# Optimization experiments

Hardware: AMD Instinct MI355X
Metric: run time of the kernel (lower is better)

The kernel has to match this reference:

```python
import jax, jax.numpy as jnp
import numpy as np

B, S, D, H = 2, 2048, 2048, 16
DH = D // H
FF = 4 * D
EPS = 1e-5


def setup_inputs() -> dict:
    key = jax.random.key(0)
    ks = jax.random.split(key, 8)
    sd = 0.02
    return {
        "hidden_states": jax.random.normal(ks[0], (B, S, D), jnp.float32),
        "ln1_w": jnp.ones((D,), jnp.float32),
        "ln1_b": jnp.zeros((D,), jnp.float32),
        "qkv_w": jax.random.normal(ks[1], (3 * D, D), jnp.float32) * sd,
        "qkv_b": jnp.zeros((3 * D,), jnp.float32),
        "dense_w": jax.random.normal(ks[2], (D, D), jnp.float32) * sd,
        "dense_b": jnp.zeros((D,), jnp.float32),
        "ln2_w": jnp.ones((D,), jnp.float32),
        "ln2_b": jnp.zeros((D,), jnp.float32),
        "fc1_w": jax.random.normal(ks[3], (FF, D), jnp.float32) * sd,
        "fc1_b": jnp.zeros((FF,), jnp.float32),
        "fc2_w": jax.random.normal(ks[4], (D, FF), jnp.float32) * sd,
        "fc2_b": jnp.zeros((D,), jnp.float32),
    }


def _layer_norm(x, w, b):
    mu = jnp.mean(x, axis=-1, keepdims=True)
    var = jnp.mean(jnp.square(x - mu), axis=-1, keepdims=True)
    return (x - mu) * jax.lax.rsqrt(var + EPS) * w + b


def _attention(x, qkv_w, qkv_b, dense_w, dense_b):
    qkv = x @ qkv_w.T + qkv_b  # [B,S,3D]
    q, k, v = jnp.split(qkv, 3, axis=-1)
    q = q.reshape(B, S, H, DH)
    k = k.reshape(B, S, H, DH)
    v = v.reshape(B, S, H, DH)
    scale = DH ** -0.5
    scores = jnp.einsum("bqhd,bkhd->bhqk", q, k) * scale
    causal = jnp.tril(jnp.ones((S, S), bool))
    scores = jnp.where(causal, scores, jnp.finfo(scores.dtype).min)
    probs = jax.nn.softmax(scores, axis=-1)
    out = jnp.einsum("bhqk,bkhd->bqhd", probs, v).reshape(B, S, D)
    return out @ dense_w.T + dense_b


def reference(hidden_states, ln1_w, ln1_b, qkv_w, qkv_b, dense_w, dense_b,
              ln2_w, ln2_b, fc1_w, fc1_b, fc2_w, fc2_b):
    residual = hidden_states
    x = _layer_norm(hidden_states, ln1_w, ln1_b)
    x = _attention(x, qkv_w, qkv_b, dense_w, dense_b) + residual
    residual = x
    h = _layer_norm(x, ln2_w, ln2_b)
    h = jax.nn.gelu(h @ fc1_w.T + fc1_b, approximate=False)
    h = h @ fc2_w.T + fc2_b
    return residual + h
```

## Files before the change

### kernel.cpp

```cpp
#include <hip/hip_runtime.h>
#include <hip/hip_bf16.h>

#define SEQ    2048
#define DMODEL 2048
#define NHEAD  16
#define DHEAD  128
#define TOK    4096
#define TD     6144
#define FFDIM  8192

typedef __attribute__((ext_vector_type(4)))  float f32x4;
typedef __attribute__((ext_vector_type(16))) float f32x16;
typedef __attribute__((ext_vector_type(8)))  short short8v;

__device__ __forceinline__ void async_ld16(const void* src, void* lds) {
  __builtin_amdgcn_global_load_lds((const __attribute__((address_space(1))) void*)src,
                                   (__attribute__((address_space(3))) void*)lds, 16, 0, 0);
}

__device__ __forceinline__ unsigned pk2(float a, float b) {
  union { __hip_bfloat16 h[2]; unsigned u; } p;
  p.h[0] = __float2bfloat16(a);
  p.h[1] = __float2bfloat16(b);
  return p.u;
}

__global__ __launch_bounds__(256) void f2bf_kernel(const float* __restrict__ in,
                                                   __hip_bfloat16* __restrict__ out, long n) {
  long i0 = ((long)blockIdx.x * 256 + threadIdx.x) * 8;
  long stride = (long)gridDim.x * 256 * 8;
  for (long i = i0; i < n; i += stride) {
    float4 a = *(const float4*)(in + i);
    float4 b = *(const float4*)(in + i + 4);
    union { __hip_bfloat16 h[8]; int4 v; } p;
    p.h[0] = __float2bfloat16(a.x); p.h[1] = __float2bfloat16(a.y);
    p.h[2] = __float2bfloat16(a.z); p.h[3] = __float2bfloat16(a.w);
    p.h[4] = __float2bfloat16(b.x); p.h[5] = __float2bfloat16(b.y);
    p.h[6] = __float2bfloat16(b.z); p.h[7] = __float2bfloat16(b.w);
    *(int4*)(out + i) = p.v;
  }
}

__global__ __launch_bounds__(256) void ln_kernel(const float* __restrict__ x,
                                                 const float* __restrict__ w,
                                                 const float* __restrict__ b,
                                                 __hip_bfloat16* __restrict__ out) {
  __shared__ float red[8];
  const int row = blockIdx.x;
  const int tid = threadIdx.x;
  const float* xr = x + (long)row * DMODEL;
  float4 v0 = ((const float4*)xr)[tid * 2];
  float4 v1 = ((const float4*)xr)[tid * 2 + 1];
  float s  = v0.x + v0.y + v0.z + v0.w + v1.x + v1.y + v1.z + v1.w;
  float ss = v0.x*v0.x + v0.y*v0.y + v0.z*v0.z + v0.w*v0.w
           + v1.x*v1.x + v1.y*v1.y + v1.z*v1.z + v1.w*v1.w;
  #pragma unroll
  for (int m = 1; m < 64; m <<= 1) { s += __shfl_xor(s, m, 64); ss += __shfl_xor(ss, m, 64); }
  if ((tid & 63) == 0) { red[tid >> 6] = s; red[4 + (tid >> 6)] = ss; }
  __syncthreads();
  s  = red[0] + red[1] + red[2] + red[3];
  ss = red[4] + red[5] + red[6] + red[7];
  const float mu = s * (1.0f / DMODEL);
  const float rs = rsqrtf(ss * (1.0f / DMODEL) - mu * mu + 1e-5f);
  float4 w0 = ((const float4*)w)[tid * 2], w1 = ((const float4*)w)[tid * 2 + 1];
  float4 b0 = ((const float4*)b)[tid * 2], b1 = ((const float4*)b)[tid * 2 + 1];
  union { __hip_bfloat16 h[8]; int4 v; } p;
  p.h[0] = __float2bfloat16((v0.x - mu) * rs * w0.x + b0.x);
  p.h[1] = __float2bfloat16((v0.y - mu) * rs * w0.y + b0.y);
  p.h[2] = __float2bfloat16((v0.z - mu) * rs * w0.z + b0.z);
  p.h[3] = __float2bfloat16((v0.w - mu) * rs * w0.w + b0.w);
  p.h[4] = __float2bfloat16((v1.x - mu) * rs * w1.x + b1.x);
  p.h[5] = __float2bfloat16((v1.y - mu) * rs * w1.y + b1.y);
  p.h[6] = __float2bfloat16((v1.z - mu) * rs * w1.z + b1.z);
  p.h[7] = __float2bfloat16((v1.w - mu) * rs * w1.w + b1.w);
  ((int4*)(out + (long)row * DMODEL))[tid] = p.v;
}

#define VMBAR(N) asm volatile("s_waitcnt vmcnt(" #N ")\ns_barrier" ::: "memory")
#define LGK(N)   do { asm volatile("s_waitcnt lgkmcnt(" #N ")" ::: "memory"); \
                      __builtin_amdgcn_sched_barrier(0); } while (0)

#define RA_READ_A(DST, BB, MH) \
  _Pragma("unroll") \
  for (int m = 0; m < 4; ++m) { \
    int row = wr * 128 + (MH) * 64 + m * 16 + l15; \
    _Pragma("unroll") \
    for (int kk = 0; kk < 2; ++kk) \
      DST[m][kk] = *(const short8v*)((BB) + row * 128 + ((((kk << 2) | c16) ^ (row & 7)) << 4)); \
  }
#define RA_READ_B(DST, BB) \
  _Pragma("unroll") \
  for (int n = 0; n < 2; ++n) { \
    int row = wc * 32 + n * 16 + l15; \
    _Pragma("unroll") \
    for (int kk = 0; kk < 2; ++kk) \
      DST[n][kk] = *(const short8v*)((BB) + 32768 + row * 128 + ((((kk << 2) | c16) ^ (row & 7)) << 4)); \
  }
#define RA_MFMA(AF, BF, MH) \
  __builtin_amdgcn_s_setprio(1); \
  _Pragma("unroll") \
  for (int m = 0; m < 4; ++m) \
    _Pragma("unroll") \
    for (int n = 0; n < 2; ++n) \
      _Pragma("unroll") \
      for (int kk = 0; kk < 2; ++kk) \
        acc[(MH) * 4 + m][n] = __builtin_amdgcn_mfma_f32_16x16x32_bf16( \
            AF[m][kk], BF[n][kk], acc[(MH) * 4 + m][n], 0, 0, 0); \
  __builtin_amdgcn_s_setprio(0);

template <int MODE>
__global__ __launch_bounds__(512, 2) void gemm128ra(const __hip_bfloat16* __restrict__ A,
                                                    const __hip_bfloat16* __restrict__ B,
                                                    const float* __restrict__ bias,
                                                    const float* __restrict__ resid,
                                                    void* __restrict__ outp,
                                                    int N, long K) {
  __shared__ __align__(16) char lds[98304];
  const int tid = threadIdx.x;
  const int lane = tid & 63, w = tid >> 6;
  const int wr = w >> 2, wc = w & 3;
  const int l15 = lane & 15, c16 = lane >> 4;
  const int gx = gridDim.x;
  const int nwg = gx * (int)gridDim.y;
  const int lin = (int)blockIdx.y * gx + (int)blockIdx.x;
  const int cpx = nwg >> 3;
  const int swz = (lin & 7) * cpx + (lin >> 3);
  const long m0 = (long)(swz / gx) * 256;
  const long n0 = (long)(swz % gx) * 128;
  const int NT = (int)(K >> 6);
  const int NI = NT >> 1;

  auto stA2 = [&](int t, int par) {
    char* base = lds + (t & 1) * 49152;
    #pragma unroll
    for (int j = 0; j < 2; ++j) {
      int q = 2 * j + par;
      int row = q * 64 + (tid >> 3);
      long col = (long)t * 64 + (((tid & 7) ^ (row & 7)) << 3);
      async_ld16(A + (m0 + row) * K + col, base + q * 8192 + w * 1024);
    }
  };
  auto stB1 = [&](int t) {
    char* base = lds + (t & 1) * 49152 + 32768;
    #pragma unroll
    for (int j = 0; j < 2; ++j) {
      int row = j * 64 + (tid >> 3);
      long col = (long)t * 64 + (((tid & 7) ^ (row & 7)) << 3);
      async_ld16(B + (n0 + row) * K + col, base + j * 8192 + w * 1024);
    }
  };

  f32x4 acc[8][2] = {};
  short8v afA[4][2], afB[4][2], bfA[2][2], bfB[2][2];
  const char* b0 = lds;
  const char* b1 = lds + 49152;

  stB1(0); stA2(0, 0); stA2(0, 1);
  stB1(1); stA2(1, 0);
  asm volatile("s_waitcnt vmcnt(4)\ns_barrier" ::: "memory");
  RA_READ_A(afA, b0, 0); RA_READ_B(bfA, b0);

  for (int i = 0; i < NI; ++i) {
    const bool last = (i == NI - 1);
    const int c = 2 * i + 1, e = 2 * i + 2, g = 2 * i + 3;

    VMBAR(4);
    RA_READ_A(afB, b0, 1);
    stA2(c, 1);
    LGK(8);
    RA_MFMA(afA, bfA, 0);

    VMBAR(2);
    RA_READ_A(afA, b1, 0);
    RA_READ_B(bfB, b1);
    if (!last) { stB1(e); stA2(e, 0); }
    LGK(12);
    RA_MFMA(afB, bfA, 1);

    if (!last) { VMBAR(4); } else { VMBAR(0); }
    RA_READ_A(afB, b1, 1);
    if (!last) stA2(e, 1);
    LGK(8);
    RA_MFMA(afA, bfB, 0);

    if (!last) {
      VMBAR(2);
      RA_READ_A(afA, b0, 0);
      RA_READ_B(bfA, b0);
      stB1(g); stA2(g, 0);
      LGK(12);
    } else {
      LGK(0);
    }
    RA_MFMA(afB, bfB, 1);
  }

  const int colq = l15;
  const int rowq = c16 * 4;
  #pragma unroll
  for (int n = 0; n < 2; ++n) {
    long col = n0 + wc * 32 + n * 16 + colq;
    float bi = bias[col];
    #pragma unroll
    for (int mi = 0; mi < 8; ++mi) {
      long row0 = m0 + wr * 128 + mi * 16 + rowq;
      #pragma unroll
      for (int j = 0; j < 4; ++j) {
        long idx = (row0 + j) * (long)N + col;
        float v = acc[mi][n][j] + bi;
        if (MODE == 0) {
          ((__hip_bfloat16*)outp)[idx] = __float2bfloat16(v);
        } else if (MODE == 1) {
          ((float*)outp)[idx] = v + resid[idx];
        } else {
          float g = 0.5f * v * (1.0f + erff(v * 0.70710678118654752f));
          ((__hip_bfloat16*)outp)[idx] = __float2bfloat16(g);
        }
      }
    }
  }
}

#define QBLK 128
#define KVB  64
#define VSTR 144
#define KBYT 16384
#define VBYT (DHEAD * VSTR)
__global__ __launch_bounds__(256, 2) void attn_kernel(const __hip_bfloat16* __restrict__ qkv,
                                                      __hip_bfloat16* __restrict__ out) {
  __shared__ __align__(16) char smem[2 * KBYT + 2 * VBYT];
  const int tid = threadIdx.x, lane = tid & 63, wid = tid >> 6;
  const int l31 = lane & 31, hi = lane >> 5;
  const int bx = blockIdx.x;
  const int bh = blockIdx.y;
  const int bb = bh >> 4, h = bh & 15;
  const long rowbase = (long)bb * SEQ;
  const int qcol = h * DHEAD, kcol = DMODEL + h * DHEAD, vcol = 2 * DMODEL + h * DHEAD;

  const int kv0s = (tid >> 4) * 4;
  const int dh0s = (tid & 15) * 8;
  auto k_stage = [&](int t) {
    char* kb = smem + (t & 1) * KBYT;
    const long kvr = rowbase + (long)t * KVB;
    #pragma unroll
    for (int i = 0; i < 4; ++i) {
      int c = i * 256 + tid;
      int row = c >> 4, slot = c & 15;
      const void* src = qkv + (kvr + row) * TD + kcol + ((slot ^ (row & 7)) << 3);
      async_ld16(src, kb + i * 4096 + wid * 1024);
    }
  };
  auto v_load = [&](int t, int4* r) {
    const long kvr = rowbase + (long)t * KVB;
    #pragma unroll
    for (int i = 0; i < 4; ++i)
      r[i] = *(const int4*)(qkv + (kvr + kv0s + i) * TD + vcol + dh0s);
  };
  auto v_write = [&](int t, const int4* r) {
    char* vt = smem + 2 * KBYT + (t & 1) * VBYT;
    union { int4 v; unsigned short s[8]; } u0, u1, u2, u3;
    u0.v = r[0]; u1.v = r[1]; u2.v = r[2]; u3.v = r[3];
    #pragma unroll
    for (int dd = 0; dd < 8; ++dd) {
      int d = (dd + ((tid >> 1) & 7)) & 7;
      unsigned lo = (unsigned)u0.s[d] | ((unsigned)u1.s[d] << 16);
      unsigned hi2 = (unsigned)u2.s[d] | ((unsigned)u3.s[d] << 16);
      uint2 wv; wv.x = lo; wv.y = hi2;
      *(uint2*)(vt + (dh0s + d) * VSTR + kv0s * 2) = wv;
    }
  };

  #pragma unroll
  for (int mem = 0; mem < 2; ++mem) {
    const int qb = mem == 0 ? (15 - bx) : bx;
    const int q0 = qb * QBLK;
    const int qw0 = q0 + wid * 32;

    short8v qf[8];
    {
      const __hip_bfloat16* qp = qkv + (rowbase + qw0 + l31) * TD + qcol + hi * 8;
      #pragma unroll
      for (int kc = 0; kc < 8; ++kc) qf[kc] = *(const short8v*)(qp + kc * 16);
    }

    f32x16 o[4] = {};
    float m_ = -1e30f, l_ = 0.0f;
    const int nt = (q0 + QBLK) / KVB;

    {
      int4 vr[4];
      v_load(0, vr);
      k_stage(0);
      v_write(0, vr);
    }
    __syncthreads();

    for (int t = 0; t < nt; ++t) {
      int4 vr[4];
      const bool more = (t + 1 < nt);
      if (more) { v_load(t + 1, vr); k_stage(t + 1); }

      const int kv0 = t * KVB;
      if (kv0 <= qw0 + 31) {
        const char* Kb = smem + (t & 1) * KBYT;
        f32x16 s0 = {}, s1 = {};
        #pragma unroll
        for (int kc = 0; kc < 8; ++kc) {
          const int colb = kc * 32 + hi * 16;
          const int r0 = l31, r1 = 32 + l31;
          short8v k0 = *(const short8v*)(Kb + r0 * 256 + (colb ^ ((r0 & 7) << 4)));
          short8v k1 = *(const short8v*)(Kb + r1 * 256 + (colb ^ ((r0 & 7) << 4)));
          s0 = __builtin_amdgcn_mfma_f32_32x32x16_bf16(k0, qf[kc], s0, 0, 0, 0);
          s1 = __builtin_amdgcn_mfma_f32_32x32x16_bf16(k1, qf[kc], s1, 0, 0, 0);
        }
        const float scale = 0.08838834764831845f;
        float sv[32];
        #pragma unroll
        for (int r = 0; r < 16; ++r) { sv[r] = s0[r] * scale; sv[16 + r] = s1[r] * scale; }
        const int qg = qw0 + l31;
        if (kv0 + KVB - 1 > qw0) {
          #pragma unroll
          for (int r = 0; r < 16; ++r) {
            int kvr_ = kv0 + (r & 3) + 8 * (r >> 2) + 4 * hi;
            if (kvr_ > qg)      sv[r]      = -1e30f;
            if (kvr_ + 32 > qg) sv[16 + r] = -1e30f;
          }
        }
        float pmax = sv[0];
        #pragma unroll
        for (int r = 1; r < 32; ++r) pmax = fmaxf(pmax, sv[r]);
        pmax = fmaxf(pmax, __shfl_xor(pmax, 32, 64));
        float mn = fmaxf(m_, pmax);
        float alpha = __expf(m_ - mn);
        m_ = mn;
        l_ *= alpha;
        #pragma unroll
        for (int d = 0; d < 4; ++d)
          #pragma unroll
          for (int r = 0; r < 16; ++r) o[d][r] *= alpha;
        float rsum = 0.0f;
        #pragma unroll
        for (int r = 0; r < 32; ++r) { sv[r] = __expf(sv[r] - m_); rsum += sv[r]; }
        l_ += rsum + __shfl_xor(rsum, 32, 64);
        int pa_[4][4];
        #pragma unroll
        for (int kc = 0; kc < 4; ++kc) {
          int ba = 16 * (kc >> 1) + 8 * (kc & 1);
          unsigned wA0 = pk2(sv[ba + 0], sv[ba + 1]);
          unsigned wA1 = pk2(sv[ba + 2], sv[ba + 3]);
          unsigned wB0 = pk2(sv[ba + 4], sv[ba + 5]);
          unsigned wB1 = pk2(sv[ba + 6], sv[ba + 7]);
          unsigned z0 = (unsigned)__shfl_xor((int)(hi ? wA0 : wB0), 32, 64);
          unsigned z1 = (unsigned)__shfl_xor((int)(hi ? wA1 : wB1), 32, 64);
          pa_[kc][0] = hi ? (int)z0 : (int)wA0;
          pa_[kc][1] = hi ? (int)z1 : (int)wA1;
          pa_[kc][2] = hi ? (int)wB0 : (int)z0;
          pa_[kc][3] = hi ? (int)wB1 : (int)z1;
        }
        const char* Vt = smem + 2 * KBYT + (t & 1) * VBYT;
        #pragma unroll
        for (int dht = 0; dht < 4; ++dht) {
          const int dh = dht * 32 + l31;
          short8v vf[4];
          #pragma unroll
          for (int kc = 0; kc < 4; ++kc)
            vf[kc] = *(const short8v*)(Vt + dh * VSTR + kc * 32 + hi * 16);
          #pragma unroll
          for (int kc = 0; kc < 4; ++kc) {
            union { int i[4]; short8v v; } bv;
            bv.i[0] = pa_[kc][0]; bv.i[1] = pa_[kc][1];
            bv.i[2] = pa_[kc][2]; bv.i[3] = pa_[kc][3];
            o[dht] = __builtin_amdgcn_mfma_f32_32x32x16_bf16(vf[kc], bv.v, o[dht], 0, 0, 0);
          }
        }
      }
      if (more) v_write(t + 1, vr);
      __syncthreads();
    }

    const float linv = 1.0f / l_;
    const long orow = (rowbase + qw0 + l31) * DMODEL + h * DHEAD;
    #pragma unroll
    for (int dht = 0; dht < 4; ++dht)
      #pragma unroll
      for (int rg = 0; rg < 4; ++rg) {
        union { __hip_bfloat16 hh[4]; uint2 u; } pk;
        #pragma unroll
        for (int i = 0; i < 4; ++i) pk.hh[i] = __float2bfloat16(o[dht][rg * 4 + i] * linv);
        *(uint2*)(out + orow + dht * 32 + 8 * rg + 4 * hi) = pk.u;
      }
  }
}

extern "C" void kernel_launch(void* const* d_in, const int* in_sizes, int n_in,
                              void* d_out, int out_size, void* d_ws, size_t ws_size,
                              hipStream_t stream) {
  const float* hidden  = (const float*)d_in[0];
  const float* ln1w    = (const float*)d_in[1];
  const float* ln1b    = (const float*)d_in[2];
  const float* qkvw    = (const float*)d_in[3];
  const float* qkvb    = (const float*)d_in[4];
  const float* densew  = (const float*)d_in[5];
  const float* denseb  = (const float*)d_in[6];
  const float* ln2w    = (const float*)d_in[7];
  const float* ln2b    = (const float*)d_in[8];
  const float* fc1w    = (const float*)d_in[9];
  const float* fc1b    = (const float*)d_in[10];
  const float* fc2w    = (const float*)d_in[11];
  const float* fc2b    = (const float*)d_in[12];

  char* ws = (char*)d_ws;
  size_t off = 0;
  auto alloc = [&](size_t bytes) { char* p = ws + off; off += (bytes + 255) & ~(size_t)255; return p; };
  __hip_bfloat16* xbf    = (__hip_bfloat16*)alloc((size_t)TOK * DMODEL * 2);
  __hip_bfloat16* wqkv   = (__hip_bfloat16*)alloc((size_t)TD * DMODEL * 2);
  __hip_bfloat16* wdense = (__hip_bfloat16*)alloc((size_t)DMODEL * DMODEL * 2);
  __hip_bfloat16* wfc1   = (__hip_bfloat16*)alloc((size_t)FFDIM * DMODEL * 2);
  __hip_bfloat16* wfc2   = (__hip_bfloat16*)alloc((size_t)DMODEL * FFDIM * 2);
  __hip_bfloat16* big    = (__hip_bfloat16*)alloc((size_t)TOK * FFDIM * 2);
  float*          x2     = (float*)alloc((size_t)TOK * DMODEL * 4);
  __hip_bfloat16* qkvbuf  = big;
  __hip_bfloat16* attnout = big + (size_t)TOK * TD;
  __hip_bfloat16* gelubuf = big;

  f2bf_kernel<<<1024, 256, 0, stream>>>(qkvw,   wqkv,   (long)TD * DMODEL);
  f2bf_kernel<<<1024, 256, 0, stream>>>(densew, wdense, (long)DMODEL * DMODEL);
  f2bf_kernel<<<1024, 256, 0, stream>>>(fc1w,   wfc1,   (long)FFDIM * DMODEL);
  f2bf_kernel<<<1024, 256, 0, stream>>>(fc2w,   wfc2,   (long)DMODEL * FFDIM);

  ln_kernel<<<TOK, 256, 0, stream>>>(hidden, ln1w, ln1b, xbf);
  gemm128ra<0><<<dim3(TD / 128, TOK / 256), 512, 0, stream>>>(xbf, wqkv, qkvb, nullptr, qkvbuf, TD, DMODEL);
  attn_kernel<<<dim3(8, 2 * NHEAD), 256, 0, stream>>>(qkvbuf, attnout);
  gemm128ra<1><<<dim3(DMODEL / 128, TOK / 256), 512, 0, stream>>>(attnout, wdense, denseb, hidden, x2, DMODEL, DMODEL);
  ln_kernel<<<TOK, 256, 0, stream>>>(x2, ln2w, ln2b, xbf);
  gemm128ra<2><<<dim3(FFDIM / 128, TOK / 256), 512, 0, stream>>>(xbf, wfc1, fc1b, nullptr, gelubuf, FFDIM, DMODEL);
  gemm128ra<1><<<dim3(DMODEL / 128, TOK / 256), 512, 0, stream>>>(gelubuf, wfc2, fc2b, x2, (float*)d_out, DMODEL, FFDIM);
}
```

Baseline: 656.9 us.

## Simplify GEMM pipeline to whole-tile double buffering with full vmcnt waits

Replaces the staggered half-tile prefetch schedule in the bf16 GEMM with a simpler double-buffer scheme. Each stage now waits for all outstanding global loads, issues the full next tile (B plus both A halves), then computes on the current buffer with a single B fragment set. This removes the interleaved partial waits and one register fragment set. In exchange, global loads overlap less finely with MFMA work, and the vmcnt(0) barriers may expose memory latency.

```diff
diff --git a/kernel.cpp b/kernel.cpp
--- a/kernel.cpp
+++ b/kernel.cpp
@@ -76,7 +76,7 @@
   ((int4*)(out + (long)row * DMODEL))[tid] = p.v;
 }
 
-#define VMBAR(N) asm volatile("s_waitcnt vmcnt(" #N ")\ns_barrier" ::: "memory")
+#define VMBAR0() asm volatile("s_waitcnt vmcnt(0)\ns_barrier" ::: "memory")
 #define LGK(N)   do { asm volatile("s_waitcnt lgkmcnt(" #N ")" ::: "memory"); \
                       __builtin_amdgcn_sched_barrier(0); } while (0)
 
@@ -109,7 +109,7 @@
   __builtin_amdgcn_s_setprio(0);
 
 template <int MODE>
-__global__ __launch_bounds__(512, 2) void gemm128ra(const __hip_bfloat16* __restrict__ A,
+__global__ __launch_bounds__(512, 2) void gemm128fr(const __hip_bfloat16* __restrict__ A,
                                                     const __hip_bfloat16* __restrict__ B,
                                                     const float* __restrict__ bias,
                                                     const float* __restrict__ resid,
@@ -151,48 +151,30 @@
   };
 
   f32x4 acc[8][2] = {};
-  short8v afA[4][2], afB[4][2], bfA[2][2], bfB[2][2];
+  short8v afA[4][2], afB[4][2], bfA[2][2];
   const char* b0 = lds;
   const char* b1 = lds + 49152;
 
   stB1(0); stA2(0, 0); stA2(0, 1);
-  stB1(1); stA2(1, 0);
-  asm volatile("s_waitcnt vmcnt(4)\ns_barrier" ::: "memory");
+  VMBAR0();
+  stB1(1); stA2(1, 0); stA2(1, 1);
   RA_READ_A(afA, b0, 0); RA_READ_B(bfA, b0);
 
   for (int i = 0; i < NI; ++i) {
-    const bool last = (i == NI - 1);
-    const int c = 2 * i + 1, e = 2 * i + 2, g = 2 * i + 3;
-
-    VMBAR(4);
     RA_READ_A(afB, b0, 1);
-    stA2(c, 1);
-    LGK(8);
-    RA_MFMA(afA, bfA, 0);
-
-    VMBAR(2);
-    RA_READ_A(afA, b1, 0);
-    RA_READ_B(bfB, b1);
-    if (!last) { stB1(e); stA2(e, 0); }
-    LGK(12);
-    RA_MFMA(afB, bfA, 1);
-
-    if (!last) { VMBAR(4); } else { VMBAR(0); }
+    LGK(8);  RA_MFMA(afA, bfA, 0);
+    LGK(0);  RA_MFMA(afB, bfA, 1);
+    VMBAR0();
+    if (2 * i + 2 < NT) { stB1(2 * i + 2); stA2(2 * i + 2, 0); stA2(2 * i + 2, 1); }
+    RA_READ_A(afA, b1, 0); RA_READ_B(bfA, b1);
     RA_READ_A(afB, b1, 1);
-    if (!last) stA2(e, 1);
-    LGK(8);
-    RA_MFMA(afA, bfB, 0);
-
-    if (!last) {
-      VMBAR(2);
-      RA_READ_A(afA, b0, 0);
-      RA_READ_B(bfA, b0);
-      stB1(g); stA2(g, 0);
-      LGK(12);
-    } else {
-      LGK(0);
-    }
-    RA_MFMA(afB, bfB, 1);
+    LGK(8);  RA_MFMA(afA, bfA, 0);
+    LGK(0);  RA_MFMA(afB, bfA, 1);
+    if (i + 1 < NI) {
+      VMBAR0();
+      stB1(2 * i + 3); stA2(2 * i + 3, 0); stA2(2 * i + 3, 1);
+      RA_READ_A(afA, b0, 0); RA_READ_B(bfA, b0);
+    }
   }
 
   const int colq = l15;
@@ -429,10 +411,10 @@
   f2bf_kernel<<<1024, 256, 0, stream>>>(fc2w,   wfc2,   (long)DMODEL * FFDIM);
 
   ln_kernel<<<TOK, 256, 0, stream>>>(hidden, ln1w, ln1b, xbf);
-  gemm128ra<0><<<dim3(TD / 128, TOK / 256), 512, 0, stream>>>(xbf, wqkv, qkvb, nullptr, qkvbuf, TD, DMODEL);
+  gemm128fr<0><<<dim3(TD / 128, TOK / 256), 512, 0, stream>>>(xbf, wqkv, qkvb, nullptr, qkvbuf, TD, DMODEL);
   attn_kernel<<<dim3(8, 2 * NHEAD), 256, 0, stream>>>(qkvbuf, attnout);
-  gemm128ra<1><<<dim3(DMODEL / 128, TOK / 256), 512, 0, stream>>>(attnout, wdense, denseb, hidden, x2, DMODEL, DMODEL);
+  gemm128fr<1><<<dim3(DMODEL / 128, TOK / 256), 512, 0, stream>>>(attnout, wdense, denseb, hidden, x2, DMODEL, DMODEL);
   ln_kernel<<<TOK, 256, 0, stream>>>(x2, ln2w, ln2b, xbf);
-  gemm128ra<2><<<dim3(FFDIM / 128, TOK / 256), 512, 0, stream>>>(xbf, wfc1, fc1b, nullptr, gelubuf, FFDIM, DMODEL);
-  gemm128ra<1><<<dim3(DMODEL / 128, TOK / 256), 512, 0, stream>>>(gelubuf, wfc2, fc2b, x2, (float*)d_out, DMODEL, FFDIM);
-}
+  gemm128fr<2><<<dim3(FFDIM / 128, TOK / 256), 512, 0, stream>>>(xbf, wfc1, fc1b, nullptr, gelubuf, FFDIM, DMODEL);
+  gemm128fr<1><<<dim3(DMODEL / 128, TOK / 256), 512, 0, stream>>>(gelubuf, wfc2, fc2b, x2, (float*)d_out, DMODEL, FFDIM);
+}
```

Measured after the change: 688.2 us. +4.8%, slower.

## Add 256x256-tile GEMM for QKV/FC1 and split-K FC2 with reduction

Applied to the files above, without the earlier changes.

Adds a new GEMM kernel with 256x256 output tiles and double-buffered 64-wide K stages, used for the QKV and FC1 projections. The larger tile is meant to raise reuse of each loaded operand. FC2 is split along K into two halves that write fp32 partials into a reused workspace region, and a separate kernel sums them with the bias and residual so the grid fills the device in one wave. The existing 128-tile kernel is also changed to reuse a single B-fragment register set, reloading it per half-step to lower register pressure. The trade-offs are 128KB of LDS per block, which limits occupancy, a simpler pipeline that waits for all loads every K step, and extra fp32 partial traffic for FC2.

```diff
diff --git a/kernel.cpp b/kernel.cpp
--- a/kernel.cpp
+++ b/kernel.cpp
@@ -76,9 +76,149 @@
   ((int4*)(out + (long)row * DMODEL))[tid] = p.v;
 }
 
+#define VMBAR0() asm volatile("s_waitcnt vmcnt(0)\ns_barrier" ::: "memory")
 #define VMBAR(N) asm volatile("s_waitcnt vmcnt(" #N ")\ns_barrier" ::: "memory")
 #define LGK(N)   do { asm volatile("s_waitcnt lgkmcnt(" #N ")" ::: "memory"); \
                       __builtin_amdgcn_sched_barrier(0); } while (0)
+
+#define R256_READ_A(BB, MH) \
+  _Pragma("unroll") \
+  for (int m = 0; m < 4; ++m) { \
+    int row = wr * 128 + (MH) * 64 + m * 16 + l15; \
+    _Pragma("unroll") \
+    for (int kk = 0; kk < 2; ++kk) \
+      af[m][kk] = *(const short8v*)((BB) + row * 128 + ((((kk << 2) | c16) ^ (row & 7)) << 4)); \
+  }
+#define R256_READ_B(NB) \
+  _Pragma("unroll") \
+  for (int n = 0; n < 2; ++n) { \
+    int row = wc * 64 + ((NB) + n) * 16 + l15; \
+    _Pragma("unroll") \
+    for (int kk = 0; kk < 2; ++kk) \
+      bf[(NB) + n][kk] = *(const short8v*)(bt + 32768 + row * 128 + ((((kk << 2) | c16) ^ (row & 7)) << 4)); \
+  }
+#define R256_MFMA(MH, NB) \
+  __builtin_amdgcn_s_setprio(1); \
+  _Pragma("unroll") \
+  for (int m = 0; m < 4; ++m) \
+    _Pragma("unroll") \
+    for (int n = 0; n < 2; ++n) \
+      _Pragma("unroll") \
+      for (int kk = 0; kk < 2; ++kk) \
+        acc[(MH) * 4 + m][(NB) + n] = __builtin_amdgcn_mfma_f32_16x16x32_bf16( \
+            af[m][kk], bf[(NB) + n][kk], acc[(MH) * 4 + m][(NB) + n], 0, 0, 0); \
+  __builtin_amdgcn_s_setprio(0);
+
+template <int MODE>
+__global__ __launch_bounds__(512, 2) void gemm256ra(const __hip_bfloat16* __restrict__ A,
+                                                    const __hip_bfloat16* __restrict__ B,
+                                                    const float* __restrict__ bias,
+                                                    float* __restrict__ pbuf,
+                                                    void* __restrict__ outp,
+                                                    int N, long Ksub, long ldk, long pstride) {
+  __shared__ __align__(16) char lds[131072];
+  const int tid = threadIdx.x;
+  const int lane = tid & 63, w = tid >> 6;
+  const int wr = w >> 2, wc = w & 3;
+  const int l15 = lane & 15, c16 = lane >> 4;
+  const int gx = gridDim.x;
+  const int nwg = gx * (int)gridDim.y;
+  const int lin = (int)blockIdx.y * gx + (int)blockIdx.x;
+  const int cpx = nwg >> 3;
+  const int swz = (lin & 7) * cpx + (lin >> 3);
+  const long m0 = (long)(swz / gx) * 256;
+  const long n0 = (long)(swz % gx) * 256;
+  const long koff = (long)blockIdx.z * Ksub;
+  const int NT = (int)(Ksub >> 6);
+
+  auto stA4 = [&](int t) {
+    char* base = lds + (t & 1) * 65536;
+    #pragma unroll
+    for (int j = 0; j < 4; ++j) {
+      int row = j * 64 + (tid >> 3);
+      long col = (long)t * 64 + (((tid & 7) ^ (row & 7)) << 3);
+      async_ld16(A + (m0 + row) * ldk + koff + col, base + j * 8192 + w * 1024);
+    }
+  };
+  auto stB4 = [&](int t) {
+    char* base = lds + (t & 1) * 65536 + 32768;
+    #pragma unroll
+    for (int j = 0; j < 4; ++j) {
+      int row = j * 64 + (tid >> 3);
+      long col = (long)t * 64 + (((tid & 7) ^ (row & 7)) << 3);
+      async_ld16(B + (n0 + row) * ldk + koff + col, base + j * 8192 + w * 1024);
+    }
+  };
+
+  f32x4 acc[8][4] = {};
+  short8v af[4][2], bf[4][2];
+
+  stA4(0); stB4(0);
+  VMBAR0();
+
+  for (int t = 0; t < NT; ++t) {
+    const char* bt = lds + (t & 1) * 65536;
+    const bool more = (t + 1 < NT);
+    if (more) stA4(t + 1);
+    R256_READ_A(bt, 0);
+    R256_READ_B(0);
+    R256_READ_B(2);
+    if (more) stB4(t + 1);
+    LGK(4);
+    R256_MFMA(0, 0);
+    LGK(0);
+    R256_MFMA(0, 2);
+    R256_READ_A(bt, 1);
+    __builtin_amdgcn_s_barrier();
+    LGK(0);
+    R256_MFMA(1, 0);
+    R256_MFMA(1, 2);
+    VMBAR0();
+  }
+
+  const int colq = l15;
+  const int rowq = c16 * 4;
+  #pragma unroll
+  for (int n = 0; n < 4; ++n) {
+    long col = n0 + wc * 64 + n * 16 + colq;
+    float bi = (MODE == 3) ? 0.0f : bias[col];
+    #pragma unroll
+    for (int mi = 0; mi < 8; ++mi) {
+      long row0 = m0 + wr * 128 + mi * 16 + rowq;
+      #pragma unroll
+      for (int j = 0; j < 4; ++j) {
+        long idx = (row0 + j) * (long)N + col;
+        float v = acc[mi][n][j] + bi;
+        if (MODE == 0) {
+          ((__hip_bfloat16*)outp)[idx] = __float2bfloat16(v);
+        } else if (MODE == 2) {
+          float g = 0.5f * v * (1.0f + erff(v * 0.70710678118654752f));
+          ((__hip_bfloat16*)outp)[idx] = __float2bfloat16(g);
+        } else {
+          pbuf[(long)blockIdx.z * pstride + idx] = v;
+        }
+      }
+    }
+  }
+}
+
+__global__ __launch_bounds__(256) void addred_kernel(const float* __restrict__ p0,
+                                                     const float* __restrict__ p1,
+                                                     const float* __restrict__ resid,
+                                                     const float* __restrict__ bias,
+                                                     float* __restrict__ out) {
+  long i = ((long)blockIdx.x * 256 + threadIdx.x) * 4;
+  float4 a = *(const float4*)(p0 + i);
+  float4 b = *(const float4*)(p1 + i);
+  float4 r = *(const float4*)(resid + i);
+  float4 bi = *(const float4*)(bias + (i & (DMODEL - 1)));
+  float4 o;
+  o.x = a.x + b.x + r.x + bi.x;
+  o.y = a.y + b.y + r.y + bi.y;
+  o.z = a.z + b.z + r.z + bi.z;
+  o.w = a.w + b.w + r.w + bi.w;
+  *(float4*)(out + i) = o;
+}
 
 #define RA_READ_A(DST, BB, MH) \
   _Pragma("unroll") \
@@ -151,48 +291,44 @@
   };
 
   f32x4 acc[8][2] = {};
-  short8v afA[4][2], afB[4][2], bfA[2][2], bfB[2][2];
+  short8v afA[4][2], afB[4][2], bfA[2][2];
   const char* b0 = lds;
   const char* b1 = lds + 49152;
 
   stB1(0); stA2(0, 0); stA2(0, 1);
   stB1(1); stA2(1, 0);
-  asm volatile("s_waitcnt vmcnt(4)\ns_barrier" ::: "memory");
-  RA_READ_A(afA, b0, 0); RA_READ_B(bfA, b0);
+  VMBAR(4);
+  RA_READ_A(afA, b0, 0);
 
   for (int i = 0; i < NI; ++i) {
     const bool last = (i == NI - 1);
     const int c = 2 * i + 1, e = 2 * i + 2, g = 2 * i + 3;
 
-    VMBAR(4);
+    RA_READ_B(bfA, b0);
     RA_READ_A(afB, b0, 1);
     stA2(c, 1);
     LGK(8);
     RA_MFMA(afA, bfA, 0);
-
     VMBAR(2);
     RA_READ_A(afA, b1, 0);
-    RA_READ_B(bfB, b1);
     if (!last) { stB1(e); stA2(e, 0); }
-    LGK(12);
+    LGK(8);
     RA_MFMA(afB, bfA, 1);
-
     if (!last) { VMBAR(4); } else { VMBAR(0); }
+    RA_READ_B(bfA, b1);
     RA_READ_A(afB, b1, 1);
     if (!last) stA2(e, 1);
     LGK(8);
-    RA_MFMA(afA, bfB, 0);
-
+    RA_MFMA(afA, bfA, 0);
     if (!last) {
       VMBAR(2);
       RA_READ_A(afA, b0, 0);
-      RA_READ_B(bfA, b0);
       stB1(g); stA2(g, 0);
-      LGK(12);
+      LGK(8);
     } else {
       LGK(0);
     }
-    RA_MFMA(afB, bfB, 1);
+    RA_MFMA(afB, bfA, 1);
   }
 
   const int colq = l15;
@@ -213,8 +349,8 @@
         } else if (MODE == 1) {
           ((float*)outp)[idx] = v + resid[idx];
         } else {
-          float g = 0.5f * v * (1.0f + erff(v * 0.70710678118654752f));
-          ((__hip_bfloat16*)outp)[idx] = __float2bfloat16(g);
+          float g2 = 0.5f * v * (1.0f + erff(v * 0.70710678118654752f));
+          ((__hip_bfloat16*)outp)[idx] = __float2bfloat16(g2);
         }
       }
     }
@@ -422,6 +558,8 @@
   __hip_bfloat16* qkvbuf  = big;
   __hip_bfloat16* attnout = big + (size_t)TOK * TD;
   __hip_bfloat16* gelubuf = big;
+  float* pbuf = (float*)xbf;
+  const long PSTRIDE = (long)TOK * DMODEL;
 
   f2bf_kernel<<<1024, 256, 0, stream>>>(qkvw,   wqkv,   (long)TD * DMODEL);
   f2bf_kernel<<<1024, 256, 0, stream>>>(densew, wdense, (long)DMODEL * DMODEL);
@@ -429,10 +567,16 @@
   f2bf_kernel<<<1024, 256, 0, stream>>>(fc2w,   wfc2,   (long)DMODEL * FFDIM);
 
   ln_kernel<<<TOK, 256, 0, stream>>>(hidden, ln1w, ln1b, xbf);
-  gemm128ra<0><<<dim3(TD / 128, TOK / 256), 512, 0, stream>>>(xbf, wqkv, qkvb, nullptr, qkvbuf, TD, DMODEL);
+  gemm256ra<0><<<dim3(TD / 256, TOK / 256, 1), 512, 0, stream>>>(
+      xbf, wqkv, qkvb, nullptr, qkvbuf, TD, DMODEL, DMODEL, 0);
   attn_kernel<<<dim3(8, 2 * NHEAD), 256, 0, stream>>>(qkvbuf, attnout);
-  gemm128ra<1><<<dim3(DMODEL / 128, TOK / 256), 512, 0, stream>>>(attnout, wdense, denseb, hidden, x2, DMODEL, DMODEL);
+  gemm128ra<1><<<dim3(DMODEL / 128, TOK / 256), 512, 0, stream>>>(
+      attnout, wdense, denseb, hidden, x2, DMODEL, DMODEL);
   ln_kernel<<<TOK, 256, 0, stream>>>(x2, ln2w, ln2b, xbf);
-  gemm128ra<2><<<dim3(FFDIM / 128, TOK / 256), 512, 0, stream>>>(xbf, wfc1, fc1b, nullptr, gelubuf, FFDIM, DMODEL);
-  gemm128ra<1><<<dim3(DMODEL / 128, TOK / 256), 512, 0, stream>>>(gelubuf, wfc2, fc2b, x2, (float*)d_out, DMODEL, FFDIM);
-}
+  gemm256ra<2><<<dim3(FFDIM / 256, TOK / 256, 1), 512, 0, stream>>>(
+      xbf, wfc1, fc1b, nullptr, gelubuf, FFDIM, DMODEL, DMODEL, 0);
+  gemm256ra<3><<<dim3(DMODEL / 256, TOK / 256, 2), 512, 0, stream>>>(
+      gelubuf, wfc2, nullptr, pbuf, nullptr, DMODEL, FFDIM / 2, FFDIM, PSTRIDE);
+  addred_kernel<<<(TOK * DMODEL) / 1024, 256, 0, stream>>>(
+      pbuf, pbuf + PSTRIDE, x2, fc2b, (float*)d_out);
+}
```

New measurement: 671.8 us. 2.3% more time.
